# Performance work log

Measured on AMD Instinct MI355X. Metric: run time of the kernel, lower is better.

## Reference

```python
import jax, jax.numpy as jnp
import numpy as np

B, T, C = 2, 1024, 2048
NH, NKV = 16, 4
HD = C // NH          # 128
NUM_REP = NH // NKV   # 4


def _apply_rotation(x, angles):
    # x: (B, T, nh, hd); angles: (T, hd//2). Equivalent to the per-pair 2x2
    # rotation matmuls in the torch code: [x0', x1'] = [[cos,-sin],[sin,cos]] @ [x0, x1]
    Bx, Tx, nh, hd = x.shape
    xp = x.reshape(Bx, Tx, nh, hd // 2, 2)
    cos = jnp.cos(angles)[None, :, None, :]  # (1, T, 1, hd//2)
    sin = jnp.sin(angles)[None, :, None, :]
    x0, x1 = xp[..., 0], xp[..., 1]
    rot = jnp.stack([cos * x0 - sin * x1, sin * x0 + cos * x1], axis=-1)
    return rot.reshape(Bx, Tx, nh, hd)


def setup_inputs() -> dict:
    key = jax.random.key(0)
    ks = jax.random.split(key, 5)
    x = jax.random.normal(ks[0], (B, T, C), dtype=jnp.float32)
    # standard RoPE angle table: pos * 10000^(-2i/hd), shape (T, hd//2)
    inv_freq = 1.0 / (10000.0 ** (jnp.arange(0, HD, 2, dtype=jnp.float32) / HD))
    angles = jnp.arange(T, dtype=jnp.float32)[:, None] * inv_freq[None, :]
    s = 0.02
    wq = jax.random.normal(ks[1], (C, C), dtype=jnp.float32) * s
    wk = jax.random.normal(ks[2], (C, NKV * HD), dtype=jnp.float32) * s
    wv = jax.random.normal(ks[3], (C, NKV * HD), dtype=jnp.float32) * s
    wo = jax.random.normal(ks[4], (C, C), dtype=jnp.float32) * s
    return {"x": x, "angles": angles, "wq": wq, "wk": wk, "wv": wv, "wo": wo}


def reference(x, angles, wq, wk, wv, wo):
    Bx, Tx, Cx = x.shape
    q = (x @ wq).reshape(Bx, Tx, NH, HD)
    k = (x @ wk).reshape(Bx, Tx, NKV, HD)
    v = (x @ wv).reshape(Bx, Tx, NKV, HD)
    q = _apply_rotation(q, angles)
    k = _apply_rotation(k, angles)
    q = q.transpose(0, 2, 1, 3)  # (B, nh, T, hd)
    k = k.transpose(0, 2, 1, 3)  # (B, nkv, T, hd)
    v = v.transpose(0, 2, 1, 3)
    if NKV != 1:
        # torch .repeat tiles kv heads: query head h uses kv head h % NKV
        k = jnp.tile(k, (1, NUM_REP, 1, 1))
        v = jnp.tile(v, (1, NUM_REP, 1, 1))
    # Faithful quirks of the source: scores = K @ Q^T (keys on rows), NO 1/sqrt(hd) scale
    scores = jnp.einsum('bhkd,bhqd->bhkq', k, q)  # (B, nh, T, T)
    mask = jnp.triu(jnp.full((Tx, Tx), -jnp.inf, dtype=scores.dtype), k=1)
    scores = scores + mask
    w = jax.nn.softmax(scores, axis=-1)
    out = jnp.einsum('bhij,bhjd->bhid', w, v)   # (B, nh, T, hd)
    out = out.transpose(0, 2, 1, 3).reshape(Bx, Tx, Cx)
    return out @ wo
```

## Files before the change

### kernel.cpp

```cpp
#include <hip/hip_runtime.h>
#include <hip/hip_bf16.h>
#include <math.h>

#define BB 2
#define TT 1024
#define CC 2048
#define NH 16
#define NKV 4
#define HD 128
#define MROWS 2048
#define QKVN 3072
#define KOFF 2048
#define VOFF 2560

typedef unsigned short u16;
typedef unsigned int   u32;
typedef _Float16 f16;
typedef _Float16 f16x8 __attribute__((ext_vector_type(8)));
typedef short    s16x8 __attribute__((ext_vector_type(8)));
typedef float    f32x4 __attribute__((ext_vector_type(4)));
typedef float    f32x16 __attribute__((ext_vector_type(16)));

__device__ __forceinline__ u16 f2h(float f) {
    union { f16 h; u16 u; } x; x.h = (f16)f; return x.u;
}
__device__ __forceinline__ float h2f(u16 u) {
    union { u16 u; f16 h; } x; x.u = u; return (float)x.h;
}

#define GLDS(gp, lp) __builtin_amdgcn_global_load_lds( \
    (const __attribute__((address_space(1))) u32*)(gp), \
    (__attribute__((address_space(3))) u32*)(lp), 16, 0, 0)

__device__ __forceinline__ void wT_tile(const float* __restrict__ src,
                                        u16* __restrict__ Wt, int Nsrc,
                                        int row_off, int idx, int t,
                                        float tile[32][33]) {
    const int k0 = (idx & 63) * 32;
    const int n0 = (idx >> 6) * 32;
    const int r = t >> 3, c4 = (t & 7) * 4;
    float4 v = *(const float4*)&src[(size_t)(k0 + r) * Nsrc + n0 + c4];
    tile[r][c4 + 0] = v.x; tile[r][c4 + 1] = v.y;
    tile[r][c4 + 2] = v.z; tile[r][c4 + 3] = v.w;
    __syncthreads();
    ushort4 o;
    o.x = f2h(tile[c4 + 0][r]); o.y = f2h(tile[c4 + 1][r]);
    o.z = f2h(tile[c4 + 2][r]); o.w = f2h(tile[c4 + 3][r]);
    *(ushort4*)&Wt[(size_t)(row_off + n0 + r) * 2048 + k0 + c4] = o;
}

__global__ __launch_bounds__(256) void prep(const float* __restrict__ x,
                                            const float* __restrict__ wq,
                                            const float* __restrict__ wk,
                                            const float* __restrict__ wv,
                                            const float* __restrict__ wo,
                                            const float* __restrict__ angles,
                                            u16* __restrict__ xb,
                                            u16* __restrict__ Wt1,
                                            u16* __restrict__ Wt2,
                                            float2* __restrict__ cs) {
    __shared__ float tile[32][33];
    const int bid = blockIdx.x, t = threadIdx.x;
    if (bid < 4096) {
        int i = bid * 256 + t;
        float4 v = ((const float4*)x)[i];
        ushort4 o;
        o.x = f2h(v.x); o.y = f2h(v.y); o.z = f2h(v.z); o.w = f2h(v.w);
        ((ushort4*)xb)[i] = o;
    } else if (bid < 8192) {
        wT_tile(wq, Wt1, 2048, 0,    bid - 4096, t, tile);
    } else if (bid < 9216) {
        wT_tile(wk, Wt1, 512,  2048, bid - 8192, t, tile);
    } else if (bid < 10240) {
        wT_tile(wv, Wt1, 512,  2560, bid - 9216, t, tile);
    } else if (bid < 14336) {
        wT_tile(wo, Wt2, 2048, 0,    bid - 10240, t, tile);
    } else {
        int i = (bid - 14336) * 256 + t;
        float a = angles[i];
        cs[i] = make_float2(cosf(a), sinf(a));
    }
}

__global__ __launch_bounds__(256) void gemm_qkv(const u16* __restrict__ A,
                                                const u16* __restrict__ Bt,
                                                u16* __restrict__ qkv,
                                                u16* __restrict__ vtg,
                                                const float2* __restrict__ cs) {
    __shared__ __align__(16) u16 As0[128 * 64];
    __shared__ __align__(16) u16 As1[128 * 64];
    __shared__ __align__(16) u16 Bs0[96 * 64];
    __shared__ __align__(16) u16 Bs1[96 * 64];
    const int t = threadIdx.x, l = t & 63, w = t >> 6;
    const int row0 = blockIdx.y * 128;
    const int col0 = blockIdx.x * 96;
    const int wr = w >> 1, wc = w & 1;
    const int lg = l >> 4, ll = l & 15;
    const int K = 2048;

    f32x4 acc[4][3] = {};

#define QSTAGE(AS, BS, k0v) do {                                              \
    _Pragma("unroll")                                                         \
    for (int e_ = 0; e_ < 4; ++e_) {                                          \
        int r_ = 32 * w + 8 * e_ + (l >> 3);                                  \
        int cg_ = (l & 7) ^ (r_ & 7);                                         \
        GLDS(A + (size_t)(row0 + r_) * K + (k0v) + cg_ * 8,                   \
             (AS) + (32 * w + 8 * e_) * 64);                                  \
    }                                                                         \
    _Pragma("unroll")                                                         \
    for (int e_ = 0; e_ < 3; ++e_) {                                          \
        int r_ = 24 * w + 8 * e_ + (l >> 3);                                  \
        int cg_ = (l & 7) ^ (r_ & 7);                                         \
        GLDS(Bt + (size_t)(col0 + r_) * K + (k0v) + cg_ * 8,                  \
             (BS) + (24 * w + 8 * e_) * 64);                                  \
    }                                                                         \
} while (0)

#define QCOMP(AS, BS) do {                                                    \
    _Pragma("unroll")                                                         \
    for (int kc_ = 0; kc_ < 2; ++kc_) {                                       \
        f16x8 af_[4], bf_[3];                                                 \
        _Pragma("unroll")                                                     \
        for (int m_ = 0; m_ < 4; ++m_) {                                      \
            int row_ = wr * 64 + 16 * m_ + ll;                                \
            af_[m_] = *(const f16x8*)&(AS)[row_ * 64 +                        \
                        (((lg + 4 * kc_) ^ (ll & 7)) * 8)];                   \
        }                                                                     \
        _Pragma("unroll")                                                     \
        for (int n_ = 0; n_ < 3; ++n_) {                                      \
            int col_ = wc * 48 + 16 * n_ + ll;                                \
            bf_[n_] = *(const f16x8*)&(BS)[col_ * 64 +                        \
                        (((lg + 4 * kc_) ^ (ll & 7)) * 8)];                   \
        }                                                                     \
        _Pragma("unroll")                                                     \
        for (int m_ = 0; m_ < 4; ++m_)                                        \
            _Pragma("unroll")                                                 \
            for (int n_ = 0; n_ < 3; ++n_)                                    \
                acc[m_][n_] = __builtin_amdgcn_mfma_f32_16x16x32_f16(         \
                    af_[m_], bf_[n_], acc[m_][n_], 0, 0, 0);                  \
    }                                                                         \
} while (0)

    QSTAGE(As0, Bs0, 0);
    __syncthreads();
#pragma unroll 1
    for (int i = 0; i < 32; i += 2) {
        QSTAGE(As1, Bs1, (i + 1) * 64);
        QCOMP(As0, Bs0);
        __syncthreads();
        if (i + 2 < 32) QSTAGE(As0, Bs0, (i + 2) * 64);
        QCOMP(As1, Bs1);
        __syncthreads();
    }
#undef QSTAGE
#undef QCOMP

    const int orow = row0 + wr * 64 + lg * 4;
    const int ocol = col0 + wc * 48 + ll;
#pragma unroll
    for (int n = 0; n < 3; ++n) {
        const int col = ocol + 16 * n;
        if (col < VOFF) {
            const int p = (col & 127) >> 1;
            const bool odd = ll & 1;
#pragma unroll
            for (int m = 0; m < 4; ++m) {
#pragma unroll
                for (int r = 0; r < 4; ++r) {
                    float v = acc[m][n][r];
                    float pr = __shfl_xor(v, 1);
                    int row = orow + 16 * m + r;
                    float2 a = cs[(row & (TT - 1)) * 64 + p];
                    float res = odd ? (a.y * pr + a.x * v) : (a.x * v - a.y * pr);
                    qkv[(size_t)row * QKVN + col] = f2h(res);
                }
            }
        } else {
            int d = col - VOFF;
            const int hk = d >> 7; d &= 127;
            const int bb = orow >> 10;
            const int base_j = orow & (TT - 1);
#pragma unroll
            for (int m = 0; m < 4; ++m) {
                ushort4 pk;
                pk.x = f2h(acc[m][n][0]); pk.y = f2h(acc[m][n][1]);
                pk.z = f2h(acc[m][n][2]); pk.w = f2h(acc[m][n][3]);
                *(ushort4*)&vtg[((size_t)(bb * NKV + hk) * 128 + d) * 1024 + base_j + 16 * m] = pk;
            }
        }
    }
}

__global__ __launch_bounds__(512) void gemm_out(const u16* __restrict__ A,
                                                const u16* __restrict__ Bt,
                                                float* __restrict__ Cf) {
    __shared__ __align__(16) u16 As0[128 * 64];
    __shared__ __align__(16) u16 As1[128 * 64];
    __shared__ __align__(16) u16 Bs0[128 * 64];
    __shared__ __align__(16) u16 Bs1[128 * 64];
    const int t = threadIdx.x, l = t & 63, w = t >> 6;
    const int row0 = blockIdx.y * 128;
    const int col0 = blockIdx.x * 128;
    const int wr = w >> 2, wc = w & 3;
    const int K = 2048;

    f32x16 acc0 = {}, acc1 = {};

#define GSTAGE(AS, BS, k0v) do {                                              \
    _Pragma("unroll")                                                         \
    for (int e_ = 0; e_ < 2; ++e_) {                                          \
        int r_ = 16 * w + 8 * e_ + (l >> 3);                                  \
        int cg_ = (l & 7) ^ (r_ & 7);                                         \
        GLDS(A  + (size_t)(row0 + r_) * K + (k0v) + cg_ * 8,                  \
             (AS) + (16 * w + 8 * e_) * 64);                                  \
        GLDS(Bt + (size_t)(col0 + r_) * K + (k0v) + cg_ * 8,                  \
             (BS) + (16 * w + 8 * e_) * 64);                                  \
    }                                                                         \
} while (0)

#define GCOMP(AS, BS) do {                                                    \
    const int rA0_ = wr * 64 + (l & 31);                                      \
    const int rA1_ = rA0_ + 32;                                               \
    const int cB_  = wc * 32 + (l & 31);                                      \
    _Pragma("unroll")                                                         \
    for (int kc_ = 0; kc_ < 4; ++kc_) {                                       \
        int c_ = 2 * kc_ + (l >> 5);                                          \
        f16x8 af0_ = *(const f16x8*)&(AS)[rA0_ * 64 + ((c_ ^ (rA0_ & 7)) * 8)]; \
        f16x8 af1_ = *(const f16x8*)&(AS)[rA1_ * 64 + ((c_ ^ (rA1_ & 7)) * 8)]; \
        f16x8 bf_  = *(const f16x8*)&(BS)[cB_  * 64 + ((c_ ^ (cB_  & 7)) * 8)]; \
        acc0 = __builtin_amdgcn_mfma_f32_32x32x16_f16(af0_, bf_, acc0, 0, 0, 0); \
        acc1 = __builtin_amdgcn_mfma_f32_32x32x16_f16(af1_, bf_, acc1, 0, 0, 0); \
    }                                                                         \
} while (0)

    GSTAGE(As0, Bs0, 0);
    __syncthreads();
#pragma unroll 1
    for (int i = 0; i < 32; i += 2) {
        GSTAGE(As1, Bs1, (i + 1) * 64);
        GCOMP(As0, Bs0);
        __syncthreads();
        if (i + 2 < 32) GSTAGE(As0, Bs0, (i + 2) * 64);
        GCOMP(As1, Bs1);
        __syncthreads();
    }
#undef GSTAGE
#undef GCOMP

    const int ocol  = col0 + wc * 32 + (l & 31);
    const int orowb = row0 + wr * 64 + 4 * (l >> 5);
#pragma unroll
    for (int reg = 0; reg < 16; ++reg) {
        int row = orowb + (reg & 3) + 8 * (reg >> 2);
        Cf[(size_t)row * CC + ocol]        = acc0[reg];
        Cf[(size_t)(row + 32) * CC + ocol] = acc1[reg];
    }
}

__global__ __launch_bounds__(512, 2) void attn_mfma(const u16* __restrict__ qkv,
                                                    const u16* __restrict__ vtg,
                                                    u16* __restrict__ attnb) {
    __shared__ __align__(16) u16 Qs0[64 * 128];
    __shared__ __align__(16) u16 Qs1[64 * 128];
    __shared__ __align__(16) u16 Vt0[128 * 64];
    __shared__ __align__(16) u16 Vt1[128 * 64];
    __shared__ __align__(16) u16 Ps[8 * 16 * 72];

    const int t = threadIdx.x, l = t & 63, w = t >> 6;
    const int bh = blockIdx.y;
    const int b = bh >> 4, h = bh & 15, hk = h & 3;
    const int lg = l >> 4, ll = l & 15;
    const int wl = w & 3;
    const int x = blockIdx.x;
    const int myIt = (w < 4) ? x : (15 - x);
    const int iw = myIt * 64 + wl * 16;

    const u16* qbase = qkv + (size_t)(b * TT) * QKVN + h * 128;
    const u16* vbase = vtg + (size_t)((b * NKV + hk) * 128) * 1024;

#define STAGE(j0v, Qd, Vd) do {                                               \
    _Pragma("unroll")                                                         \
    for (int e_ = 0; e_ < 2; ++e_) {                                          \
        int r_ = 4 * (2 * w + e_) + (l >> 4);                                 \
        GLDS(qbase + (size_t)((j0v) + r_) * QKVN +                            \
                 (((l & 15) ^ (r_ & 7)) * 8),                                 \
             (Qd) + 4 * (2 * w + e_) * 128);                                  \
        int d_ = 8 * (2 * w + e_) + (l >> 3);                                 \
        GLDS(vbase + (size_t)d_ * 1024 + (j0v) + (((l & 7) ^ (d_ & 7)) * 8),  \
             (Vd) + 8 * (2 * w + e_) * 64);                                   \
    }                                                                         \
} while (0)

    f16x8 kf[4];
    {
        const u16* kp = qkv + (size_t)(b * TT + iw + ll) * QKVN + KOFF + hk * 128 + lg * 8;
#pragma unroll
        for (int c = 0; c < 4; ++c) kf[c] = *(const f16x8*)(kp + 32 * c);
    }

    f32x4 o[8] = {};
    float mrun[4] = {-1e30f, -1e30f, -1e30f, -1e30f};
    float lrun[4] = {0.f, 0.f, 0.f, 0.f};

    const int nt = 16 - x;
    STAGE(0, Qs0, Vt0);
    __syncthreads();

#pragma unroll 1
    for (int jt = 0; jt < nt; ++jt) {
        u16* Qc = (jt & 1) ? Qs1 : Qs0;
        u16* Vc = (jt & 1) ? Vt1 : Vt0;
        if (jt + 1 < nt) {
            u16* Qn = (jt & 1) ? Qs0 : Qs1;
            u16* Vn = (jt & 1) ? Vt0 : Vt1;
            STAGE((jt + 1) * 64, Qn, Vn);
        }

        if (jt <= myIt) {
            f32x4 s[4] = {};
#pragma unroll
            for (int kc = 0; kc < 4; ++kc)
#pragma unroll
                for (int n = 0; n < 4; ++n) {
                    f16x8 qf = *(const f16x8*)&Qc[(16 * n + ll) * 128 + (((lg + 4 * kc) ^ (ll & 7)) * 8)];
                    s[n] = __builtin_amdgcn_mfma_f32_16x16x32_f16(kf[kc], qf, s[n], 0, 0, 0);
                }

            if (jt == myIt) {
#pragma unroll
                for (int n = 0; n < 4; ++n)
#pragma unroll
                    for (int r = 0; r < 4; ++r)
                        s[n][r] = (16 * n + ll <= 16 * wl + 4 * lg + r) ? s[n][r] : -1e30f;
            }

            float tml[4];
            bool need = false;
#pragma unroll
            for (int r = 0; r < 4; ++r) {
                float tm = fmaxf(fmaxf(s[0][r], s[1][r]), fmaxf(s[2][r], s[3][r]));
                tml[r] = tm;
                need |= (tm > mrun[r] + 8.0f);
            }
            if (__any(need)) {
#pragma unroll
                for (int r = 0; r < 4; ++r) {
                    float tm = tml[r];
                    tm = fmaxf(tm, __shfl_xor(tm, 1, 16));
                    tm = fmaxf(tm, __shfl_xor(tm, 2, 16));
                    tm = fmaxf(tm, __shfl_xor(tm, 4, 16));
                    tm = fmaxf(tm, __shfl_xor(tm, 8, 16));
                    float mnew = fmaxf(mrun[r], tm);
                    float al = __expf(mrun[r] - mnew);
                    lrun[r] *= al;
                    mrun[r] = mnew;
#pragma unroll
                    for (int n = 0; n < 8; ++n) o[n][r] *= al;
                }
            }
            float p[4][4];
#pragma unroll
            for (int r = 0; r < 4; ++r) {
                float ps = 0.f;
#pragma unroll
                for (int n = 0; n < 4; ++n) { p[n][r] = __expf(s[n][r] - mrun[r]); ps += p[n][r]; }
                lrun[r] += ps;
            }

            u16* pw = Ps + w * (16 * 72);
#pragma unroll
            for (int n = 0; n < 4; ++n)
#pragma unroll
                for (int r = 0; r < 4; ++r)
                    pw[(4 * lg + r) * 72 + ll + 16 * n] = f2h(p[n][r]);
            f16x8 pa0 = *(const f16x8*)&pw[ll * 72 + 8 * lg];
            f16x8 pa1 = *(const f16x8*)&pw[ll * 72 + 8 * lg + 32];

#pragma unroll
            for (int n = 0; n < 8; ++n) {
                f16x8 vf0 = *(const f16x8*)&Vc[(16 * n + ll) * 64 + ((lg ^ (ll & 7)) * 8)];
                o[n] = __builtin_amdgcn_mfma_f32_16x16x32_f16(pa0, vf0, o[n], 0, 0, 0);
                f16x8 vf1 = *(const f16x8*)&Vc[(16 * n + ll) * 64 + (((lg + 4) ^ (ll & 7)) * 8)];
                o[n] = __builtin_amdgcn_mfma_f32_16x16x32_f16(pa1, vf1, o[n], 0, 0, 0);
            }
        }

        __syncthreads();
    }

    u16* dst = attnb + (size_t)(b * TT + iw + 4 * lg) * CC + h * 128 + ll;
#pragma unroll
    for (int r = 0; r < 4; ++r) {
        float L = lrun[r];
        L += __shfl_xor(L, 1, 16);
        L += __shfl_xor(L, 2, 16);
        L += __shfl_xor(L, 4, 16);
        L += __shfl_xor(L, 8, 16);
        float inv = 1.0f / L;
#pragma unroll
        for (int n = 0; n < 8; ++n)
            dst[(size_t)r * CC + 16 * n] = f2h(o[n][r] * inv);
    }
#undef STAGE
}

extern "C" void kernel_launch(void* const* d_in, const int* in_sizes, int n_in,
                              void* d_out, int out_size, void* d_ws, size_t ws_size,
                              hipStream_t stream) {
    const float* x      = (const float*)d_in[0];
    const float* angles = (const float*)d_in[1];
    const float* wq     = (const float*)d_in[2];
    const float* wk     = (const float*)d_in[3];
    const float* wv     = (const float*)d_in[4];
    const float* wo     = (const float*)d_in[5];
    float* out = (float*)d_out;

    char* ws = (char*)d_ws;
    u16*    Wt1   = (u16*)ws;
    u16*    Wt2   = (u16*)(ws + 12582912);
    float2* cs    = (float2*)(ws + 20971520);
    u16*    xb    = (u16*)(ws + 21495808);
    u16*    qkvb  = (u16*)(ws + 29884416);
    u16*    vtg   = (u16*)(ws + 42467328);
    u16*    attnb = (u16*)(ws + 44564480);

    prep<<<14592, 256, 0, stream>>>(x, wq, wk, wv, wo, angles, xb, Wt1, Wt2, cs);
    gemm_qkv<<<dim3(32, 16), 256, 0, stream>>>(xb, Wt1, qkvb, vtg, cs);
    attn_mfma<<<dim3(8, BB * NH), 512, 0, stream>>>(qkvb, vtg, attnb);
    gemm_out<<<dim3(16, 16), 512, 0, stream>>>(attnb, Wt2, out);
}
```

Baseline: 113.6 us.

## Unify QKV and output GEMMs on 128x64 tiles with 32x32 MFMA

Both projection GEMMs now share one staging and compute macro that uses 128x64 tiles, 4 waves per block and 32x32x16 MFMA, in place of 128x96 tiles with 16x16 MFMA for QKV and 128x128 tiles with 8 waves for the output GEMM. The grids grow to 48x16 and 32x16 blocks, and occupancy is hinted with launch_bounds(256,3). The aim is better MFMA efficiency and more blocks to fill the CUs. The RoPE and V-transpose epilogue is rewritten to match the 32x32 accumulator layout. The attention kernel also raises wave priority around its MFMA sections via s_setprio.

```diff
diff --git a/kernel.cpp b/kernel.cpp
--- a/kernel.cpp
+++ b/kernel.cpp
@@ -82,179 +82,143 @@
     }
 }
 
-__global__ __launch_bounds__(256) void gemm_qkv(const u16* __restrict__ A,
-                                                const u16* __restrict__ Bt,
-                                                u16* __restrict__ qkv,
-                                                u16* __restrict__ vtg,
-                                                const float2* __restrict__ cs) {
-    __shared__ __align__(16) u16 As0[128 * 64];
-    __shared__ __align__(16) u16 As1[128 * 64];
-    __shared__ __align__(16) u16 Bs0[96 * 64];
-    __shared__ __align__(16) u16 Bs1[96 * 64];
-    const int t = threadIdx.x, l = t & 63, w = t >> 6;
-    const int row0 = blockIdx.y * 128;
-    const int col0 = blockIdx.x * 96;
-    const int wr = w >> 1, wc = w & 1;
-    const int lg = l >> 4, ll = l & 15;
-    const int K = 2048;
-
-    f32x4 acc[4][3] = {};
-
-#define QSTAGE(AS, BS, k0v) do {                                              \
+
+#define USTAGE(A_, Bt_, AS, BS, k0v, K_) do {                                 \
     _Pragma("unroll")                                                         \
     for (int e_ = 0; e_ < 4; ++e_) {                                          \
         int r_ = 32 * w + 8 * e_ + (l >> 3);                                  \
-        int cg_ = (l & 7) ^ (r_ & 7);                                         \
-        GLDS(A + (size_t)(row0 + r_) * K + (k0v) + cg_ * 8,                   \
+        GLDS(A_ + (size_t)(row0 + r_) * K_ + (k0v) +                          \
+                 (((l & 7) ^ (r_ & 7)) * 8),                                  \
              (AS) + (32 * w + 8 * e_) * 64);                                  \
     }                                                                         \
     _Pragma("unroll")                                                         \
-    for (int e_ = 0; e_ < 3; ++e_) {                                          \
-        int r_ = 24 * w + 8 * e_ + (l >> 3);                                  \
-        int cg_ = (l & 7) ^ (r_ & 7);                                         \
-        GLDS(Bt + (size_t)(col0 + r_) * K + (k0v) + cg_ * 8,                  \
-             (BS) + (24 * w + 8 * e_) * 64);                                  \
-    }                                                                         \
-} while (0)
-
-#define QCOMP(AS, BS) do {                                                    \
-    _Pragma("unroll")                                                         \
-    for (int kc_ = 0; kc_ < 2; ++kc_) {                                       \
-        f16x8 af_[4], bf_[3];                                                 \
-        _Pragma("unroll")                                                     \
-        for (int m_ = 0; m_ < 4; ++m_) {                                      \
-            int row_ = wr * 64 + 16 * m_ + ll;                                \
-            af_[m_] = *(const f16x8*)&(AS)[row_ * 64 +                        \
-                        (((lg + 4 * kc_) ^ (ll & 7)) * 8)];                   \
-        }                                                                     \
-        _Pragma("unroll")                                                     \
-        for (int n_ = 0; n_ < 3; ++n_) {                                      \
-            int col_ = wc * 48 + 16 * n_ + ll;                                \
-            bf_[n_] = *(const f16x8*)&(BS)[col_ * 64 +                        \
-                        (((lg + 4 * kc_) ^ (ll & 7)) * 8)];                   \
-        }                                                                     \
-        _Pragma("unroll")                                                     \
-        for (int m_ = 0; m_ < 4; ++m_)                                        \
-            _Pragma("unroll")                                                 \
-            for (int n_ = 0; n_ < 3; ++n_)                                    \
-                acc[m_][n_] = __builtin_amdgcn_mfma_f32_16x16x32_f16(         \
-                    af_[m_], bf_[n_], acc[m_][n_], 0, 0, 0);                  \
-    }                                                                         \
-} while (0)
-
-    QSTAGE(As0, Bs0, 0);
-    __syncthreads();
-#pragma unroll 1
-    for (int i = 0; i < 32; i += 2) {
-        QSTAGE(As1, Bs1, (i + 1) * 64);
-        QCOMP(As0, Bs0);
-        __syncthreads();
-        if (i + 2 < 32) QSTAGE(As0, Bs0, (i + 2) * 64);
-        QCOMP(As1, Bs1);
-        __syncthreads();
-    }
-#undef QSTAGE
-#undef QCOMP
-
-    const int orow = row0 + wr * 64 + lg * 4;
-    const int ocol = col0 + wc * 48 + ll;
-#pragma unroll
-    for (int n = 0; n < 3; ++n) {
-        const int col = ocol + 16 * n;
-        if (col < VOFF) {
-            const int p = (col & 127) >> 1;
-            const bool odd = ll & 1;
-#pragma unroll
-            for (int m = 0; m < 4; ++m) {
-#pragma unroll
-                for (int r = 0; r < 4; ++r) {
-                    float v = acc[m][n][r];
-                    float pr = __shfl_xor(v, 1);
-                    int row = orow + 16 * m + r;
-                    float2 a = cs[(row & (TT - 1)) * 64 + p];
-                    float res = odd ? (a.y * pr + a.x * v) : (a.x * v - a.y * pr);
-                    qkv[(size_t)row * QKVN + col] = f2h(res);
-                }
-            }
-        } else {
-            int d = col - VOFF;
-            const int hk = d >> 7; d &= 127;
-            const int bb = orow >> 10;
-            const int base_j = orow & (TT - 1);
-#pragma unroll
-            for (int m = 0; m < 4; ++m) {
-                ushort4 pk;
-                pk.x = f2h(acc[m][n][0]); pk.y = f2h(acc[m][n][1]);
-                pk.z = f2h(acc[m][n][2]); pk.w = f2h(acc[m][n][3]);
-                *(ushort4*)&vtg[((size_t)(bb * NKV + hk) * 128 + d) * 1024 + base_j + 16 * m] = pk;
-            }
-        }
-    }
-}
-
-__global__ __launch_bounds__(512) void gemm_out(const u16* __restrict__ A,
-                                                const u16* __restrict__ Bt,
-                                                float* __restrict__ Cf) {
-    __shared__ __align__(16) u16 As0[128 * 64];
-    __shared__ __align__(16) u16 As1[128 * 64];
-    __shared__ __align__(16) u16 Bs0[128 * 64];
-    __shared__ __align__(16) u16 Bs1[128 * 64];
-    const int t = threadIdx.x, l = t & 63, w = t >> 6;
-    const int row0 = blockIdx.y * 128;
-    const int col0 = blockIdx.x * 128;
-    const int wr = w >> 2, wc = w & 3;
-    const int K = 2048;
-
-    f32x16 acc0 = {}, acc1 = {};
-
-#define GSTAGE(AS, BS, k0v) do {                                              \
-    _Pragma("unroll")                                                         \
     for (int e_ = 0; e_ < 2; ++e_) {                                          \
         int r_ = 16 * w + 8 * e_ + (l >> 3);                                  \
-        int cg_ = (l & 7) ^ (r_ & 7);                                         \
-        GLDS(A  + (size_t)(row0 + r_) * K + (k0v) + cg_ * 8,                  \
-             (AS) + (16 * w + 8 * e_) * 64);                                  \
-        GLDS(Bt + (size_t)(col0 + r_) * K + (k0v) + cg_ * 8,                  \
+        GLDS(Bt_ + (size_t)(col0 + r_) * K_ + (k0v) +                         \
+                  (((l & 7) ^ (r_ & 7)) * 8),                                 \
              (BS) + (16 * w + 8 * e_) * 64);                                  \
     }                                                                         \
 } while (0)
 
-#define GCOMP(AS, BS) do {                                                    \
+#define UCOMP(AS, BS) do {                                                    \
     const int rA0_ = wr * 64 + (l & 31);                                      \
     const int rA1_ = rA0_ + 32;                                               \
     const int cB_  = wc * 32 + (l & 31);                                      \
     _Pragma("unroll")                                                         \
     for (int kc_ = 0; kc_ < 4; ++kc_) {                                       \
         int c_ = 2 * kc_ + (l >> 5);                                          \
+        f16x8 bf_  = *(const f16x8*)&(BS)[cB_  * 64 + ((c_ ^ (cB_  & 7)) * 8)]; \
         f16x8 af0_ = *(const f16x8*)&(AS)[rA0_ * 64 + ((c_ ^ (rA0_ & 7)) * 8)]; \
+        acc0 = __builtin_amdgcn_mfma_f32_32x32x16_f16(af0_, bf_, acc0, 0, 0, 0); \
         f16x8 af1_ = *(const f16x8*)&(AS)[rA1_ * 64 + ((c_ ^ (rA1_ & 7)) * 8)]; \
-        f16x8 bf_  = *(const f16x8*)&(BS)[cB_  * 64 + ((c_ ^ (cB_  & 7)) * 8)]; \
-        acc0 = __builtin_amdgcn_mfma_f32_32x32x16_f16(af0_, bf_, acc0, 0, 0, 0); \
         acc1 = __builtin_amdgcn_mfma_f32_32x32x16_f16(af1_, bf_, acc1, 0, 0, 0); \
     }                                                                         \
 } while (0)
 
-    GSTAGE(As0, Bs0, 0);
+__global__ __launch_bounds__(256, 3) void gemm_qkv(const u16* __restrict__ A,
+                                                   const u16* __restrict__ Bt,
+                                                   u16* __restrict__ qkv,
+                                                   u16* __restrict__ vtg,
+                                                   const float2* __restrict__ cs) {
+    __shared__ __align__(16) u16 As0[128 * 64];
+    __shared__ __align__(16) u16 As1[128 * 64];
+    __shared__ __align__(16) u16 Bs0[64 * 64];
+    __shared__ __align__(16) u16 Bs1[64 * 64];
+    const int t = threadIdx.x, l = t & 63, w = t >> 6;
+    const int row0 = blockIdx.y * 128;
+    const int col0 = blockIdx.x * 64;
+    const int wr = w >> 1, wc = w & 1;
+    const int K = 2048;
+
+    f32x16 acc0 = {}, acc1 = {};
+
+    USTAGE(A, Bt, As0, Bs0, 0, K);
     __syncthreads();
 #pragma unroll 1
     for (int i = 0; i < 32; i += 2) {
-        GSTAGE(As1, Bs1, (i + 1) * 64);
-        GCOMP(As0, Bs0);
+        USTAGE(A, Bt, As1, Bs1, (i + 1) * 64, K);
+        UCOMP(As0, Bs0);
         __syncthreads();
-        if (i + 2 < 32) GSTAGE(As0, Bs0, (i + 2) * 64);
-        GCOMP(As1, Bs1);
+        if (i + 2 < 32) USTAGE(A, Bt, As0, Bs0, (i + 2) * 64, K);
+        UCOMP(As1, Bs1);
         __syncthreads();
     }
-#undef GSTAGE
-#undef GCOMP
-
-    const int ocol  = col0 + wc * 32 + (l & 31);
-    const int orowb = row0 + wr * 64 + 4 * (l >> 5);
-#pragma unroll
-    for (int reg = 0; reg < 16; ++reg) {
-        int row = orowb + (reg & 3) + 8 * (reg >> 2);
-        Cf[(size_t)row * CC + ocol]        = acc0[reg];
-        Cf[(size_t)(row + 32) * CC + ocol] = acc1[reg];
+
+    const int ocol = col0 + wc * 32 + (l & 31);
+    const int orow_base = row0 + wr * 64 + 4 * (l >> 5);
+    if (ocol < VOFF) {
+        const int p = (ocol & 127) >> 1;
+        const bool odd = l & 1;
+#pragma unroll
+        for (int s = 0; s < 2; ++s) {
+            const f32x16 av = s ? acc1 : acc0;
+#pragma unroll
+            for (int reg = 0; reg < 16; ++reg) {
+                float v = av[reg];
+                float pr = __shfl_xor(v, 1);
+                int row = orow_base + 32 * s + (reg & 3) + 8 * (reg >> 2);
+                float2 a = cs[(row & (TT - 1)) * 64 + p];
+                float res = odd ? (a.y * pr + a.x * v) : (a.x * v - a.y * pr);
+                qkv[(size_t)row * QKVN + ocol] = f2h(res);
+            }
+        }
+    } else {
+        int d = ocol - VOFF;
+        const int hk = d >> 7; d &= 127;
+        const int bb = row0 >> 10;
+        u16* vrow = vtg + ((size_t)(bb * NKV + hk) * 128 + d) * 1024;
+#pragma unroll
+        for (int s = 0; s < 2; ++s) {
+            const f32x16 av = s ? acc1 : acc0;
+#pragma unroll
+            for (int g = 0; g < 4; ++g) {
+                ushort4 pk;
+                pk.x = f2h(av[4 * g + 0]); pk.y = f2h(av[4 * g + 1]);
+                pk.z = f2h(av[4 * g + 2]); pk.w = f2h(av[4 * g + 3]);
+                int j = (orow_base + 32 * s + 8 * g) & (TT - 1);
+                *(ushort4*)&vrow[j] = pk;
+            }
+        }
+    }
+}
+
+__global__ __launch_bounds__(256, 3) void gemm_out(const u16* __restrict__ A,
+                                                   const u16* __restrict__ Bt,
+                                                   float* __restrict__ Cf) {
+    __shared__ __align__(16) u16 As0[128 * 64];
+    __shared__ __align__(16) u16 As1[128 * 64];
+    __shared__ __align__(16) u16 Bs0[64 * 64];
+    __shared__ __align__(16) u16 Bs1[64 * 64];
+    const int t = threadIdx.x, l = t & 63, w = t >> 6;
+    const int row0 = blockIdx.y * 128;
+    const int col0 = blockIdx.x * 64;
+    const int wr = w >> 1, wc = w & 1;
+    const int K = 2048;
+
+    f32x16 acc0 = {}, acc1 = {};
+
+    USTAGE(A, Bt, As0, Bs0, 0, K);
+    __syncthreads();
+#pragma unroll 1
+    for (int i = 0; i < 32; i += 2) {
+        USTAGE(A, Bt, As1, Bs1, (i + 1) * 64, K);
+        UCOMP(As0, Bs0);
+        __syncthreads();
+        if (i + 2 < 32) USTAGE(A, Bt, As0, Bs0, (i + 2) * 64, K);
+        UCOMP(As1, Bs1);
+        __syncthreads();
+    }
+
+    const int ocol = col0 + wc * 32 + (l & 31);
+    const int orow_base = row0 + wr * 64 + 4 * (l >> 5);
+#pragma unroll
+    for (int s = 0; s < 2; ++s) {
+        const f32x16 av = s ? acc1 : acc0;
+#pragma unroll
+        for (int reg = 0; reg < 16; ++reg) {
+            int row = orow_base + 32 * s + (reg & 3) + 8 * (reg >> 2);
+            Cf[(size_t)row * CC + ocol] = av[reg];
+        }
     }
 }
 
@@ -319,6 +283,7 @@
 
         if (jt <= myIt) {
             f32x4 s[4] = {};
+            __builtin_amdgcn_s_setprio(1);
 #pragma unroll
             for (int kc = 0; kc < 4; ++kc)
 #pragma unroll
@@ -326,6 +291,7 @@
                     f16x8 qf = *(const f16x8*)&Qc[(16 * n + ll) * 128 + (((lg + 4 * kc) ^ (ll & 7)) * 8)];
                     s[n] = __builtin_amdgcn_mfma_f32_16x16x32_f16(kf[kc], qf, s[n], 0, 0, 0);
                 }
+            __builtin_amdgcn_s_setprio(0);
 
             if (jt == myIt) {
 #pragma unroll
@@ -377,6 +343,7 @@
             f16x8 pa0 = *(const f16x8*)&pw[ll * 72 + 8 * lg];
             f16x8 pa1 = *(const f16x8*)&pw[ll * 72 + 8 * lg + 32];
 
+            __builtin_amdgcn_s_setprio(1);
 #pragma unroll
             for (int n = 0; n < 8; ++n) {
                 f16x8 vf0 = *(const f16x8*)&Vc[(16 * n + ll) * 64 + ((lg ^ (ll & 7)) * 8)];
@@ -384,6 +351,7 @@
                 f16x8 vf1 = *(const f16x8*)&Vc[(16 * n + ll) * 64 + (((lg + 4) ^ (ll & 7)) * 8)];
                 o[n] = __builtin_amdgcn_mfma_f32_16x16x32_f16(pa1, vf1, o[n], 0, 0, 0);
             }
+            __builtin_amdgcn_s_setprio(0);
         }
 
         __syncthreads();
@@ -426,7 +394,7 @@
     u16*    attnb = (u16*)(ws + 44564480);
 
     prep<<<14592, 256, 0, stream>>>(x, wq, wk, wv, wo, angles, xb, Wt1, Wt2, cs);
-    gemm_qkv<<<dim3(32, 16), 256, 0, stream>>>(xb, Wt1, qkvb, vtg, cs);
+    gemm_qkv<<<dim3(48, 16), 256, 0, stream>>>(xb, Wt1, qkvb, vtg, cs);
     attn_mfma<<<dim3(8, BB * NH), 512, 0, stream>>>(qkvb, vtg, attnb);
-    gemm_out<<<dim3(16, 16), 512, 0, stream>>>(attnb, Wt2, out);
-}
+    gemm_out<<<dim3(32, 16), 256, 0, stream>>>(attnb, Wt2, out);
+}
```

After: 117.6 us. +3.5%, slower.
